# Kernel tuning notes

Hardware: AMD Instinct MI355X
Metric: run time of the kernel (lower is better)

Reference implementation:

```python
import jax, jax.numpy as jnp
import numpy as np
import math

MODEL_DIM = 1024
NUM_HEADS = 16
ATTN_DIM = MODEL_DIM // NUM_HEADS  # 64
ROWS, COLS, AXES = 32, 32, 2
PAIRS = ATTN_DIM // (AXES * 2)     # 16
BATCH = 4
TOKENS = ROWS * COLS               # 1024


def setup_inputs() -> dict:
    key = jax.random.key(0)
    ks = jax.random.split(key, 8)
    s = 1.0 / math.sqrt(MODEL_DIM)
    return {
        "x": jax.random.normal(ks[0], (BATCH, TOKENS, MODEL_DIM), jnp.float32),
        "cos": jax.random.uniform(ks[1], (ROWS, COLS, AXES, PAIRS), jnp.float32),
        "sin": jax.random.uniform(ks[2], (ROWS, COLS, AXES, PAIRS), jnp.float32),
        "Wq": jax.random.normal(ks[3], (MODEL_DIM, MODEL_DIM), jnp.float32) * s,
        "Wk": jax.random.normal(ks[4], (MODEL_DIM, MODEL_DIM), jnp.float32) * s,
        "Wv": jax.random.normal(ks[5], (MODEL_DIM, MODEL_DIM), jnp.float32) * s,
        "Wo": jax.random.normal(ks[6], (MODEL_DIM, MODEL_DIM), jnp.float32) * s,
        "bo": jax.random.normal(ks[7], (MODEL_DIM,), jnp.float32) * 0.01,
    }


def _apply_rope(W, cos, sin):
    # W: (b, h, tokens, attn_dim) -> (b, h, rows, cols, axes, pairs, 2)
    b, h, n, d = W.shape
    rows, cols, axes, pairs = cos.shape
    Wp = W.reshape(b, h, rows, cols, axes, pairs, 2)
    c = cos[None, None]
    s = sin[None, None]
    w0, w1 = Wp[..., 0], Wp[..., 1]
    out = jnp.stack([c * w0 - s * w1, s * w0 + c * w1], axis=-1)
    return out.reshape(b, h, n, d)


def reference(x, cos, sin, Wq, Wk, Wv, Wo, bo):
    b, n, _ = x.shape
    # torch Linear: y = x @ W.T
    Q = (x @ Wq.T).reshape(b, n, NUM_HEADS, ATTN_DIM).transpose(0, 2, 1, 3)
    K = (x @ Wk.T).reshape(b, n, NUM_HEADS, ATTN_DIM).transpose(0, 2, 1, 3)
    V = (x @ Wv.T).reshape(b, n, NUM_HEADS, ATTN_DIM).transpose(0, 2, 1, 3)
    Q = _apply_rope(Q, cos, sin)
    K = _apply_rope(K, cos, sin)
    scores = jnp.einsum("bhqd,bhkd->bhqk", Q, K) / math.sqrt(ATTN_DIM)
    attn = jax.nn.softmax(scores, axis=-1)
    o = jnp.einsum("bhqk,bhkd->bhqd", attn, V)
    o = o.transpose(0, 2, 1, 3).reshape(b, n, MODEL_DIM)
    return o @ Wo.T + bo
```

## Files before the change

### kernel.cpp

```cpp
#include <hip/hip_runtime.h>
#include <hip/hip_bf16.h>

typedef __bf16 bf16;
typedef __bf16 bf16x4 __attribute__((ext_vector_type(4)));
typedef __bf16 bf16x8 __attribute__((ext_vector_type(8)));
typedef float  f32x4  __attribute__((ext_vector_type(4)));
typedef unsigned int u32x2 __attribute__((ext_vector_type(2)));

#define MFMA16(a, b, c) __builtin_amdgcn_mfma_f32_16x16x32_bf16((a), (b), (c), 0, 0, 0)

#define GLOBAL_AS(p) ((const __attribute__((address_space(1))) void*)(p))
#define LDS_AS(p)    ((__attribute__((address_space(3))) void*)(p))

#define BATCH 4
#define TOK   1024
#define DIM   1024
#define HEADS 16
#define HD    64
#define MTOT  (BATCH * TOK)
#define MELEM (1024u * 1024u)

__global__ __launch_bounds__(256) void k_cast(const float* __restrict__ X,
                                              bf16* __restrict__ xh)
{
    size_t i0 = ((size_t)blockIdx.x * 256 + threadIdx.x) * 8;
    f32x4 a = *(const f32x4*)(X + i0);
    f32x4 b = *(const f32x4*)(X + i0 + 4);
    bf16x8 h;
    #pragma unroll
    for (int j = 0; j < 4; j++) { h[j] = (bf16)a[j]; h[4 + j] = (bf16)b[j]; }
    *(bf16x8*)(xh + i0) = h;
}

__global__ __launch_bounds__(256) void k_split(
    const float* __restrict__ W0, const float* __restrict__ W1,
    const float* __restrict__ W2, const float* __restrict__ W3,
    bf16* __restrict__ wsp)
{
    const int widx = blockIdx.y;
    const float* W = (widx == 0) ? W0 : (widx == 1) ? W1 : (widx == 2) ? W2 : W3;
    size_t i0 = ((size_t)blockIdx.x * 256 + threadIdx.x) * 8;
    f32x4 a = *(const f32x4*)(W + i0);
    f32x4 b = *(const f32x4*)(W + i0 + 4);
    bf16x8 h, l;
    #pragma unroll
    for (int j = 0; j < 4; j++) {
        bf16 g0 = (bf16)a[j]; h[j] = g0;     l[j] = (bf16)(a[j] - (float)g0);
        bf16 g1 = (bf16)b[j]; h[4 + j] = g1; l[4 + j] = (bf16)(b[j] - (float)g1);
    }
    *(bf16x8*)(wsp + (size_t)widx * MELEM + i0) = h;
    if (widx == 3)
        *(bf16x8*)(wsp + 4 * (size_t)MELEM + i0) = l;
}

__global__ __launch_bounds__(512) void k_gemmQKV(
    const bf16* __restrict__ Ag, const bf16* __restrict__ wsp,
    const float* __restrict__ cosT, const float* __restrict__ sinT,
    bf16* __restrict__ q_o, bf16* __restrict__ k_o, bf16* __restrict__ v_o)
{
    __shared__ bf16 Alin[128 * 64];
    __shared__ bf16 Blin[256 * 64];

    const int fid = blockIdx.x;
    const int swz = (fid & 7) * 48 + (fid >> 3);
    const int nt = swz % 12;
    const int mt = swz / 12;

    const int t = threadIdx.x;
    const int lane = t & 63;
    const int w = t >> 6;
    const int wr = w >> 2, wc = w & 3;
    const int l15 = lane & 15;

    f32x4 acc[4][4];
    #pragma unroll
    for (int m = 0; m < 4; m++)
        #pragma unroll
        for (int n = 0; n < 4; n++)
            #pragma unroll
            for (int r = 0; r < 4; r++) acc[m][n][r] = 0.f;

    const int srow = lane >> 3;
    const int schk8 = ((lane & 7) ^ (srow & 7)) * 8;
    const bf16* asrc = Ag  + (size_t)(mt * 128 + srow) * DIM + schk8;
    const bf16* bsrc = wsp + (size_t)(nt * 256 + srow) * DIM + schk8;

    for (int k0 = 0; k0 < DIM; k0 += 64) {
        __syncthreads();
        #pragma unroll
        for (int ii = 0; ii < 2; ++ii) {
            int i = w * 2 + ii;
            __builtin_amdgcn_global_load_lds(
                GLOBAL_AS(asrc + (size_t)i * 8 * DIM + k0),
                LDS_AS(&Alin[i * 512]), 16, 0, 0);
        }
        #pragma unroll
        for (int jj = 0; jj < 4; ++jj) {
            int j = w * 4 + jj;
            __builtin_amdgcn_global_load_lds(
                GLOBAL_AS(bsrc + (size_t)j * 8 * DIM + k0),
                LDS_AS(&Blin[j * 512]), 16, 0, 0);
        }
        __syncthreads();

        #pragma unroll
        for (int ks = 0; ks < 2; ks++) {
            const int cc = (lane >> 4) + ks * 4;
            bf16x8 fb[4];
            #pragma unroll
            for (int n = 0; n < 4; n++) {
                int rb = wc * 64 + n * 16 + l15;
                fb[n] = *(const bf16x8*)&Blin[rb * 64 + ((cc ^ (rb & 7)) << 3)];
            }
            #pragma unroll
            for (int m = 0; m < 4; m++) {
                int r = wr * 64 + m * 16 + l15;
                bf16x8 fa = *(const bf16x8*)&Alin[r * 64 + ((cc ^ (r & 7)) << 3)];
                #pragma unroll
                for (int n = 0; n < 4; n++)
                    acc[m][n] = MFMA16(fa, fb[n], acc[m][n]);
            }
        }
    }

    const int mode = nt >> 2;
    const int h = (nt & 3) * 4 + wc;
    if (mode == 2) {
        #pragma unroll
        for (int m = 0; m < 4; m++) {
            const int grow0 = mt * 128 + wr * 64 + m * 16 + (lane >> 4) * 4;
            const int b = grow0 >> 10, ntok0 = grow0 & (TOK - 1);
            #pragma unroll
            for (int n = 0; n < 4; n++) {
                const int d = n * 16 + l15;
                bf16x4 pk;
                #pragma unroll
                for (int r = 0; r < 4; r++) pk[r] = (bf16)acc[m][n][r];
                *(bf16x4*)&v_o[((size_t)((b * HEADS + h) * HD + d)) * TOK + ntok0] = pk;
            }
        }
    } else {
        __syncthreads();
        float* cosL = (float*)Alin;
        float* sinL = (float*)Blin;
        const int tb = (mt & 7) * 128;
        *(f32x4*)(cosL + t * 8)     = *(const f32x4*)(cosT + (size_t)tb * 32 + t * 8);
        *(f32x4*)(cosL + t * 8 + 4) = *(const f32x4*)(cosT + (size_t)tb * 32 + t * 8 + 4);
        *(f32x4*)(sinL + t * 8)     = *(const f32x4*)(sinT + (size_t)tb * 32 + t * 8);
        *(f32x4*)(sinL + t * 8 + 4) = *(const f32x4*)(sinT + (size_t)tb * 32 + t * 8 + 4);
        __syncthreads();

        bf16* dst = (mode == 0) ? q_o : k_o;
        const float sc = (mode == 0) ? 0.125f : 1.0f;
        #pragma unroll
        for (int m = 0; m < 4; m++) {
            const int grow0 = mt * 128 + wr * 64 + m * 16 + (lane >> 4) * 4;
            const int b = grow0 >> 10, ntok0 = grow0 & (TOK - 1);
            const int loc0 = wr * 64 + m * 16 + (lane >> 4) * 4;
            #pragma unroll
            for (int n = 0; n < 4; n++) {
                const int d = n * 16 + l15;
                const int idp = (d >> 5) * 16 + ((d >> 1) & 15);
                const bool ev = (d & 1) == 0;
                #pragma unroll
                for (int r = 0; r < 4; r++) {
                    float v = acc[m][n][r];
                    float pr = __shfl_xor(v, 1, 64);
                    float c = cosL[(loc0 + r) * 32 + idp];
                    float s = sinL[(loc0 + r) * 32 + idp];
                    float res = (ev ? (c * v - s * pr) : (s * pr + c * v)) * sc;
                    dst[((size_t)(b * HEADS + h) * TOK + ntok0 + r) * HD + d] = (bf16)res;
                }
            }
        }
    }
}

__global__ __launch_bounds__(256) void k_gemmO(
    const bf16* __restrict__ Ag, const bf16* __restrict__ wsp,
    const float* __restrict__ bo, float* __restrict__ f_o)
{
    __shared__ bf16 Alin[128 * 64];
    __shared__ bf16 Bhlin[128 * 64];
    __shared__ bf16 Bllin[128 * 64];

    const bf16* Bh_g = wsp + 3 * (size_t)MELEM;
    const bf16* Bl_g = wsp + 4 * (size_t)MELEM;

    const int fid = blockIdx.x;
    const int swz = (fid & 7) * 32 + (fid >> 3);
    const int nt = swz & 7;
    const int mt = swz >> 3;

    const int t = threadIdx.x;
    const int lane = t & 63;
    const int w = t >> 6;
    const int wr = w >> 1, wc = w & 1;

    f32x4 acc[4][4];
    #pragma unroll
    for (int m = 0; m < 4; m++)
        #pragma unroll
        for (int n = 0; n < 4; n++)
            #pragma unroll
            for (int r = 0; r < 4; r++) acc[m][n][r] = 0.f;

    const int srow = lane >> 3;
    const int schk8 = ((lane & 7) ^ (srow & 7)) * 8;
    const bf16* asrc  = Ag   + (size_t)(mt * 128 + srow) * DIM + schk8;
    const bf16* bhsrc = Bh_g + (size_t)(nt * 128 + srow) * DIM + schk8;
    const bf16* blsrc = Bl_g + (size_t)(nt * 128 + srow) * DIM + schk8;

    for (int k0 = 0; k0 < DIM; k0 += 64) {
        __syncthreads();
        #pragma unroll
        for (int ii = 0; ii < 4; ++ii) {
            int i = w * 4 + ii;
            size_t roff = (size_t)i * 8 * DIM + k0;
            __builtin_amdgcn_global_load_lds(GLOBAL_AS(asrc + roff),
                                             LDS_AS(&Alin[i * 512]), 16, 0, 0);
            __builtin_amdgcn_global_load_lds(GLOBAL_AS(bhsrc + roff),
                                             LDS_AS(&Bhlin[i * 512]), 16, 0, 0);
            __builtin_amdgcn_global_load_lds(GLOBAL_AS(blsrc + roff),
                                             LDS_AS(&Bllin[i * 512]), 16, 0, 0);
        }
        __syncthreads();

        const int l15 = lane & 15;
        #pragma unroll
        for (int ks = 0; ks < 2; ks++) {
            const int cc = (lane >> 4) + ks * 4;
            bf16x8 fbh[4], fbl[4];
            #pragma unroll
            for (int n = 0; n < 4; n++) {
                int r = wc * 64 + n * 16 + l15;
                int off = r * 64 + ((cc ^ (r & 7)) << 3);
                fbh[n] = *(const bf16x8*)&Bhlin[off];
                fbl[n] = *(const bf16x8*)&Bllin[off];
            }
            #pragma unroll
            for (int m = 0; m < 4; m++) {
                int r = wr * 64 + m * 16 + l15;
                bf16x8 fa = *(const bf16x8*)&Alin[r * 64 + ((cc ^ (r & 7)) << 3)];
                #pragma unroll
                for (int n = 0; n < 4; n++) {
                    acc[m][n] = MFMA16(fa, fbh[n], acc[m][n]);
                    acc[m][n] = MFMA16(fa, fbl[n], acc[m][n]);
                }
            }
        }
    }

    #pragma unroll
    for (int m = 0; m < 4; m++) {
        #pragma unroll
        for (int n = 0; n < 4; n++) {
            const int grow0 = mt * 128 + wr * 64 + m * 16 + (lane >> 4) * 4;
            const int gcol  = nt * 128 + wc * 64 + n * 16 + (lane & 15);
            const float bias = bo[gcol];
            #pragma unroll
            for (int r = 0; r < 4; r++)
                f_o[(size_t)(grow0 + r) * DIM + gcol] = acc[m][n][r] + bias;
        }
    }
}

__global__ __launch_bounds__(256) void k_attn(
    const bf16* __restrict__ Q, const bf16* __restrict__ K,
    const bf16* __restrict__ Vt, bf16* __restrict__ O)
{
    __shared__ bf16 Ks[128 * 64];
    __shared__ bf16 Vs[64 * 128];
    __shared__ bf16 Ps[64 * 128];

    const int fid = blockIdx.x;
    const int swz = (fid & 7) * 128 + (fid >> 3);
    const int qt = swz & 15;
    const int bh = swz >> 4;

    const int t = threadIdx.x;
    const int lane = t & 63;
    const int w = t >> 6;
    const int col = lane & 15;
    const int grp = lane >> 4;

    const bf16* qp = Q + ((size_t)bh * TOK + qt * 64 + w * 16 + col) * HD + grp * 8;
    bf16x8 qf0 = *(const bf16x8*)qp;
    bf16x8 qf1 = *(const bf16x8*)(qp + 32);

    const bf16* ksrc = K + ((size_t)bh * TOK + (lane >> 3)) * HD
                         + (size_t)(((lane & 7) ^ ((lane >> 3) & 7)) * 8);
    const bf16* vbase = Vt + ((size_t)bh * HD + grp) * TOK;
    const bf16* vsrc_e = vbase + (size_t)(((lane & 15) ^ grp) * 8);
    const bf16* vsrc_o = vbase + (size_t)(((lane & 15) ^ (grp + 4)) * 8);

    float l_sum = 0.f;
    f32x4 zero = {0.f, 0.f, 0.f, 0.f};
    f32x4 o_[4];
    #pragma unroll
    for (int dt = 0; dt < 4; dt++) o_[dt] = zero;

    unsigned int* PsU = (unsigned int*)Ps;
    const int m7 = col & 7;

    for (int kt = 0; kt < 8; kt++) {
        __syncthreads();
        #pragma unroll
        for (int ii = 0; ii < 4; ++ii) {
            int i = w * 4 + ii;
            __builtin_amdgcn_global_load_lds(
                GLOBAL_AS(ksrc + (size_t)(kt * 128 + i * 8) * HD),
                LDS_AS(&Ks[i * 512]), 16, 0, 0);
            const bf16* vs = (i & 1) ? vsrc_o : vsrc_e;
            __builtin_amdgcn_global_load_lds(
                GLOBAL_AS(vs + (size_t)i * 4 * TOK + kt * 128),
                LDS_AS(&Vs[i * 512]), 16, 0, 0);
        }
        __syncthreads();

        f32x4 s[8];
        #pragma unroll
        for (int ct = 0; ct < 8; ct++) s[ct] = zero;
        #pragma unroll
        for (int ct = 0; ct < 8; ct++) {
            int rbase = (ct * 16 + col) * 64;
            bf16x8 kf0 = *(const bf16x8*)&Ks[rbase + ((grp ^ m7) << 3)];
            bf16x8 kf1 = *(const bf16x8*)&Ks[rbase + (((grp + 4) ^ m7) << 3)];
            s[ct] = MFMA16(kf0, qf0, s[ct]);
            s[ct] = MFMA16(kf1, qf1, s[ct]);
        }

        const int qrow = w * 16 + col;
        #pragma unroll
        for (int ct = 0; ct < 8; ct++) {
            float p0 = exp2f(s[ct][0] * 1.44269504f - 23.0831206f);
            float p1 = exp2f(s[ct][1] * 1.44269504f - 23.0831206f);
            float p2 = exp2f(s[ct][2] * 1.44269504f - 23.0831206f);
            float p3 = exp2f(s[ct][3] * 1.44269504f - 23.0831206f);
            l_sum += (p0 + p1) + (p2 + p3);
            unsigned int a0, a1;
            asm("v_cvt_pk_bf16_f32 %0, %1, %2" : "=v"(a0) : "v"(p0), "v"(p1));
            asm("v_cvt_pk_bf16_f32 %0, %1, %2" : "=v"(a1) : "v"(p2), "v"(p3));
            int cs = (2 * ct + (grp >> 1)) ^ m7;
            u32x2 st = {a0, a1};
            *(u32x2*)&PsU[qrow * 64 + cs * 4 + (grp & 1) * 2] = st;
        }

        #pragma unroll
        for (int tt = 0; tt < 4; tt++) {
            bf16x8 pf = *(const bf16x8*)&Ps[qrow * 128 + (((4 * tt + grp) ^ m7) << 3)];
            #pragma unroll
            for (int dt = 0; dt < 4; dt++) {
                bf16x8 vf = *(const bf16x8*)&Vs[(dt * 16 + col) * 128
                                                + (((4 * tt + grp) ^ m7) << 3)];
                o_[dt] = MFMA16(vf, pf, o_[dt]);
            }
        }
    }

    l_sum += __shfl_xor(l_sum, 16, 64);
    l_sum += __shfl_xor(l_sum, 32, 64);
    const float inv = 1.0f / l_sum;

    const int b = bh >> 4, h = bh & 15;
    const int ntok = qt * 64 + w * 16 + col;
    #pragma unroll
    for (int dt = 0; dt < 4; dt++) {
        bf16x4 pk4;
        #pragma unroll
        for (int r = 0; r < 4; r++) pk4[r] = (bf16)(o_[dt][r] * inv);
        *(bf16x4*)&O[((size_t)b * TOK + ntok) * DIM + h * HD + dt * 16 + grp * 4] = pk4;
    }
}

extern "C" void kernel_launch(void* const* d_in, const int* in_sizes, int n_in,
                              void* d_out, int out_size, void* d_ws, size_t ws_size,
                              hipStream_t stream)
{
    const float* x    = (const float*)d_in[0];
    const float* cosT = (const float*)d_in[1];
    const float* sinT = (const float*)d_in[2];
    const float* Wq   = (const float*)d_in[3];
    const float* Wk   = (const float*)d_in[4];
    const float* Wv   = (const float*)d_in[5];
    const float* Wo   = (const float*)d_in[6];
    const float* bo   = (const float*)d_in[7];
    float* out = (float*)d_out;

    bf16* xh  = (bf16*)d_ws;
    bf16* qw  = xh + 4 * (size_t)MELEM;
    bf16* kw  = qw + 4 * (size_t)MELEM;
    bf16* vw  = kw + 4 * (size_t)MELEM;
    bf16* wsp = vw + 4 * (size_t)MELEM;
    bf16* ow  = xh;

    k_cast<<<dim3(2048), dim3(256), 0, stream>>>(x, xh);
    k_split<<<dim3(512, 4), dim3(256), 0, stream>>>(Wq, Wk, Wv, Wo, wsp);
    k_gemmQKV<<<dim3(384), dim3(512), 0, stream>>>(xh, wsp, cosT, sinT, qw, kw, vw);
    k_attn<<<dim3(1024), dim3(256), 0, stream>>>(qw, kw, vw, ow);
    k_gemmO<<<dim3(256), dim3(256), 0, stream>>>(ow, wsp, bo, out);
}
```

Baseline: 114.3 us.

## Double attention query tile per block and merge cast/split prep kernels

```diff
diff --git a/kernel.cpp b/kernel.cpp
--- a/kernel.cpp
+++ b/kernel.cpp
@@ -20,37 +20,39 @@
 #define MTOT  (BATCH * TOK)
 #define MELEM (1024u * 1024u)
 
-__global__ __launch_bounds__(256) void k_cast(const float* __restrict__ X,
-                                              bf16* __restrict__ xh)
-{
-    size_t i0 = ((size_t)blockIdx.x * 256 + threadIdx.x) * 8;
-    f32x4 a = *(const f32x4*)(X + i0);
-    f32x4 b = *(const f32x4*)(X + i0 + 4);
-    bf16x8 h;
-    #pragma unroll
-    for (int j = 0; j < 4; j++) { h[j] = (bf16)a[j]; h[4 + j] = (bf16)b[j]; }
-    *(bf16x8*)(xh + i0) = h;
-}
-
-__global__ __launch_bounds__(256) void k_split(
+__global__ __launch_bounds__(256) void k_prep(
+    const float* __restrict__ X,
     const float* __restrict__ W0, const float* __restrict__ W1,
     const float* __restrict__ W2, const float* __restrict__ W3,
-    bf16* __restrict__ wsp)
+    bf16* __restrict__ xh, bf16* __restrict__ wsp)
 {
-    const int widx = blockIdx.y;
-    const float* W = (widx == 0) ? W0 : (widx == 1) ? W1 : (widx == 2) ? W2 : W3;
-    size_t i0 = ((size_t)blockIdx.x * 256 + threadIdx.x) * 8;
-    f32x4 a = *(const f32x4*)(W + i0);
-    f32x4 b = *(const f32x4*)(W + i0 + 4);
-    bf16x8 h, l;
-    #pragma unroll
-    for (int j = 0; j < 4; j++) {
-        bf16 g0 = (bf16)a[j]; h[j] = g0;     l[j] = (bf16)(a[j] - (float)g0);
-        bf16 g1 = (bf16)b[j]; h[4 + j] = g1; l[4 + j] = (bf16)(b[j] - (float)g1);
-    }
-    *(bf16x8*)(wsp + (size_t)widx * MELEM + i0) = h;
-    if (widx == 3)
-        *(bf16x8*)(wsp + 4 * (size_t)MELEM + i0) = l;
+    const int bid = blockIdx.x;
+    if (bid < 2048) {
+        size_t i0 = ((size_t)bid * 256 + threadIdx.x) * 8;
+        f32x4 a = *(const f32x4*)(X + i0);
+        f32x4 b = *(const f32x4*)(X + i0 + 4);
+        bf16x8 h;
+        #pragma unroll
+        for (int j = 0; j < 4; j++) { h[j] = (bf16)a[j]; h[4 + j] = (bf16)b[j]; }
+        *(bf16x8*)(xh + i0) = h;
+    } else {
+        const int b2 = bid - 2048;
+        const int widx = b2 >> 9;
+        const int inner = b2 & 511;
+        const float* W = (widx == 0) ? W0 : (widx == 1) ? W1 : (widx == 2) ? W2 : W3;
+        size_t i0 = ((size_t)inner * 256 + threadIdx.x) * 8;
+        f32x4 a = *(const f32x4*)(W + i0);
+        f32x4 b = *(const f32x4*)(W + i0 + 4);
+        bf16x8 h, l;
+        #pragma unroll
+        for (int j = 0; j < 4; j++) {
+            bf16 g0 = (bf16)a[j]; h[j] = g0;     l[j] = (bf16)(a[j] - (float)g0);
+            bf16 g1 = (bf16)b[j]; h[4 + j] = g1; l[4 + j] = (bf16)(b[j] - (float)g1);
+        }
+        *(bf16x8*)(wsp + (size_t)widx * MELEM + i0) = h;
+        if (widx == 3)
+            *(bf16x8*)(wsp + 4 * (size_t)MELEM + i0) = l;
+    }
 }
 
 __global__ __launch_bounds__(512) void k_gemmQKV(
@@ -271,22 +273,26 @@
 {
     __shared__ bf16 Ks[128 * 64];
     __shared__ bf16 Vs[64 * 128];
-    __shared__ bf16 Ps[64 * 128];
+    __shared__ bf16 Ps[128 * 128];
 
     const int fid = blockIdx.x;
-    const int swz = (fid & 7) * 128 + (fid >> 3);
-    const int qt = swz & 15;
-    const int bh = swz >> 4;
+    const int swz = (fid & 7) * 64 + (fid >> 3);
+    const int qt = swz & 7;
+    const int bh = swz >> 3;
 
     const int t = threadIdx.x;
     const int lane = t & 63;
     const int w = t >> 6;
     const int col = lane & 15;
     const int grp = lane >> 4;
-
-    const bf16* qp = Q + ((size_t)bh * TOK + qt * 64 + w * 16 + col) * HD + grp * 8;
-    bf16x8 qf0 = *(const bf16x8*)qp;
-    bf16x8 qf1 = *(const bf16x8*)(qp + 32);
+    const int m7 = col & 7;
+    const int qrow = w * 16 + col;
+
+    const bf16* qp0 = Q + ((size_t)bh * TOK + qt * 128 + qrow) * HD + grp * 8;
+    bf16x8 qa0 = *(const bf16x8*)qp0;
+    bf16x8 qb0 = *(const bf16x8*)(qp0 + 32);
+    bf16x8 qa1 = *(const bf16x8*)(qp0 + 64 * HD);
+    bf16x8 qb1 = *(const bf16x8*)(qp0 + 64 * HD + 32);
 
     const bf16* ksrc = K + ((size_t)bh * TOK + (lane >> 3)) * HD
                          + (size_t)(((lane & 7) ^ ((lane >> 3) & 7)) * 8);
@@ -294,14 +300,13 @@
     const bf16* vsrc_e = vbase + (size_t)(((lane & 15) ^ grp) * 8);
     const bf16* vsrc_o = vbase + (size_t)(((lane & 15) ^ (grp + 4)) * 8);
 
-    float l_sum = 0.f;
+    float l0 = 0.f, l1 = 0.f;
     f32x4 zero = {0.f, 0.f, 0.f, 0.f};
-    f32x4 o_[4];
+    f32x4 oA[4], oB[4];
     #pragma unroll
-    for (int dt = 0; dt < 4; dt++) o_[dt] = zero;
+    for (int dt = 0; dt < 4; dt++) { oA[dt] = zero; oB[dt] = zero; }
 
     unsigned int* PsU = (unsigned int*)Ps;
-    const int m7 = col & 7;
 
     for (int kt = 0; kt < 8; kt++) {
         __syncthreads();
@@ -318,58 +323,94 @@
         }
         __syncthreads();
 
-        f32x4 s[8];
-        #pragma unroll
-        for (int ct = 0; ct < 8; ct++) s[ct] = zero;
-        #pragma unroll
-        for (int ct = 0; ct < 8; ct++) {
-            int rbase = (ct * 16 + col) * 64;
-            bf16x8 kf0 = *(const bf16x8*)&Ks[rbase + ((grp ^ m7) << 3)];
-            bf16x8 kf1 = *(const bf16x8*)&Ks[rbase + (((grp + 4) ^ m7) << 3)];
-            s[ct] = MFMA16(kf0, qf0, s[ct]);
-            s[ct] = MFMA16(kf1, qf1, s[ct]);
-        }
-
-        const int qrow = w * 16 + col;
-        #pragma unroll
-        for (int ct = 0; ct < 8; ct++) {
-            float p0 = exp2f(s[ct][0] * 1.44269504f - 23.0831206f);
-            float p1 = exp2f(s[ct][1] * 1.44269504f - 23.0831206f);
-            float p2 = exp2f(s[ct][2] * 1.44269504f - 23.0831206f);
-            float p3 = exp2f(s[ct][3] * 1.44269504f - 23.0831206f);
-            l_sum += (p0 + p1) + (p2 + p3);
-            unsigned int a0, a1;
-            asm("v_cvt_pk_bf16_f32 %0, %1, %2" : "=v"(a0) : "v"(p0), "v"(p1));
-            asm("v_cvt_pk_bf16_f32 %0, %1, %2" : "=v"(a1) : "v"(p2), "v"(p3));
-            int cs = (2 * ct + (grp >> 1)) ^ m7;
-            u32x2 st = {a0, a1};
-            *(u32x2*)&PsU[qrow * 64 + cs * 4 + (grp & 1) * 2] = st;
+        {
+            f32x4 s[8];
+            #pragma unroll
+            for (int ct = 0; ct < 8; ct++) s[ct] = zero;
+            #pragma unroll
+            for (int ct = 0; ct < 8; ct++) {
+                int rbase = (ct * 16 + col) * 64;
+                bf16x8 kf0 = *(const bf16x8*)&Ks[rbase + ((grp ^ m7) << 3)];
+                bf16x8 kf1 = *(const bf16x8*)&Ks[rbase + (((grp + 4) ^ m7) << 3)];
+                s[ct] = MFMA16(kf0, qa0, s[ct]);
+                s[ct] = MFMA16(kf1, qb0, s[ct]);
+            }
+            #pragma unroll
+            for (int ct = 0; ct < 8; ct++) {
+                float p0 = exp2f(s[ct][0] * 1.44269504f - 23.0831206f);
+                float p1 = exp2f(s[ct][1] * 1.44269504f - 23.0831206f);
+                float p2 = exp2f(s[ct][2] * 1.44269504f - 23.0831206f);
+                float p3 = exp2f(s[ct][3] * 1.44269504f - 23.0831206f);
+                l0 += (p0 + p1) + (p2 + p3);
+                unsigned int a0, a1;
+                asm("v_cvt_pk_bf16_f32 %0, %1, %2" : "=v"(a0) : "v"(p0), "v"(p1));
+                asm("v_cvt_pk_bf16_f32 %0, %1, %2" : "=v"(a1) : "v"(p2), "v"(p3));
+                int cs = (2 * ct + (grp >> 1)) ^ m7;
+                u32x2 st = {a0, a1};
+                *(u32x2*)&PsU[qrow * 64 + cs * 4 + (grp & 1) * 2] = st;
+            }
+        }
+        {
+            f32x4 s[8];
+            #pragma unroll
+            for (int ct = 0; ct < 8; ct++) s[ct] = zero;
+            #pragma unroll
+            for (int ct = 0; ct < 8; ct++) {
+                int rbase = (ct * 16 + col) * 64;
+                bf16x8 kf0 = *(const bf16x8*)&Ks[rbase + ((grp ^ m7) << 3)];
+                bf16x8 kf1 = *(const bf16x8*)&Ks[rbase + (((grp + 4) ^ m7) << 3)];
+                s[ct] = MFMA16(kf0, qa1, s[ct]);
+                s[ct] = MFMA16(kf1, qb1, s[ct]);
+            }
+            #pragma unroll
+            for (int ct = 0; ct < 8; ct++) {
+                float p0 = exp2f(s[ct][0] * 1.44269504f - 23.0831206f);
+                float p1 = exp2f(s[ct][1] * 1.44269504f - 23.0831206f);
+                float p2 = exp2f(s[ct][2] * 1.44269504f - 23.0831206f);
+                float p3 = exp2f(s[ct][3] * 1.44269504f - 23.0831206f);
+                l1 += (p0 + p1) + (p2 + p3);
+                unsigned int a0, a1;
+                asm("v_cvt_pk_bf16_f32 %0, %1, %2" : "=v"(a0) : "v"(p0), "v"(p1));
+                asm("v_cvt_pk_bf16_f32 %0, %1, %2" : "=v"(a1) : "v"(p2), "v"(p3));
+                int cs = (2 * ct + (grp >> 1)) ^ m7;
+                u32x2 st = {a0, a1};
+                *(u32x2*)&PsU[(64 + qrow) * 64 + cs * 4 + (grp & 1) * 2] = st;
+            }
         }
 
         #pragma unroll
         for (int tt = 0; tt < 4; tt++) {
-            bf16x8 pf = *(const bf16x8*)&Ps[qrow * 128 + (((4 * tt + grp) ^ m7) << 3)];
+            const int coff = ((4 * tt + grp) ^ m7) << 3;
+            bf16x8 pfA = *(const bf16x8*)&Ps[qrow * 128 + coff];
+            bf16x8 pfB = *(const bf16x8*)&Ps[(64 + qrow) * 128 + coff];
             #pragma unroll
             for (int dt = 0; dt < 4; dt++) {
-                bf16x8 vf = *(const bf16x8*)&Vs[(dt * 16 + col) * 128
-                                                + (((4 * tt + grp) ^ m7) << 3)];
-                o_[dt] = MFMA16(vf, pf, o_[dt]);
-            }
-        }
-    }
-
-    l_sum += __shfl_xor(l_sum, 16, 64);
-    l_sum += __shfl_xor(l_sum, 32, 64);
-    const float inv = 1.0f / l_sum;
+                bf16x8 vf = *(const bf16x8*)&Vs[(dt * 16 + col) * 128 + coff];
+                oA[dt] = MFMA16(vf, pfA, oA[dt]);
+                oB[dt] = MFMA16(vf, pfB, oB[dt]);
+            }
+        }
+    }
+
+    l0 += __shfl_xor(l0, 16, 64);
+    l0 += __shfl_xor(l0, 32, 64);
+    l1 += __shfl_xor(l1, 16, 64);
+    l1 += __shfl_xor(l1, 32, 64);
+    const float inv0 = 1.0f / l0;
+    const float inv1 = 1.0f / l1;
 
     const int b = bh >> 4, h = bh & 15;
-    const int ntok = qt * 64 + w * 16 + col;
+    const int nt0 = qt * 128 + qrow;
     #pragma unroll
     for (int dt = 0; dt < 4; dt++) {
-        bf16x4 pk4;
-        #pragma unroll
-        for (int r = 0; r < 4; r++) pk4[r] = (bf16)(o_[dt][r] * inv);
-        *(bf16x4*)&O[((size_t)b * TOK + ntok) * DIM + h * HD + dt * 16 + grp * 4] = pk4;
+        bf16x4 pkA, pkB;
+        #pragma unroll
+        for (int r = 0; r < 4; r++) {
+            pkA[r] = (bf16)(oA[dt][r] * inv0);
+            pkB[r] = (bf16)(oB[dt][r] * inv1);
+        }
+        *(bf16x4*)&O[((size_t)b * TOK + nt0) * DIM + h * HD + dt * 16 + grp * 4] = pkA;
+        *(bf16x4*)&O[((size_t)b * TOK + nt0 + 64) * DIM + h * HD + dt * 16 + grp * 4] = pkB;
     }
 }
 
@@ -394,9 +435,8 @@
     bf16* wsp = vw + 4 * (size_t)MELEM;
     bf16* ow  = xh;
 
-    k_cast<<<dim3(2048), dim3(256), 0, stream>>>(x, xh);
-    k_split<<<dim3(512, 4), dim3(256), 0, stream>>>(Wq, Wk, Wv, Wo, wsp);
+    k_prep<<<dim3(4096), dim3(256), 0, stream>>>(x, Wq, Wk, Wv, Wo, xh, wsp);
     k_gemmQKV<<<dim3(384), dim3(512), 0, stream>>>(xh, wsp, cosT, sinT, qw, kw, vw);
-    k_attn<<<dim3(1024), dim3(256), 0, stream>>>(qw, kw, vw, ow);
+    k_attn<<<dim3(512), dim3(256), 0, stream>>>(qw, kw, vw, ow);
     k_gemmO<<<dim3(256), dim3(256), 0, stream>>>(ow, wsp, bo, out);
 }
```

New measurement: 107.1 us. 1.07x faster.

## Double-buffer K/V tiles in attention and merge cast/split prep kernels

Applied to the files above, without the earlier changes.

```diff
diff --git a/kernel.cpp b/kernel.cpp
--- a/kernel.cpp
+++ b/kernel.cpp
@@ -20,37 +20,39 @@
 #define MTOT  (BATCH * TOK)
 #define MELEM (1024u * 1024u)
 
-__global__ __launch_bounds__(256) void k_cast(const float* __restrict__ X,
-                                              bf16* __restrict__ xh)
-{
-    size_t i0 = ((size_t)blockIdx.x * 256 + threadIdx.x) * 8;
-    f32x4 a = *(const f32x4*)(X + i0);
-    f32x4 b = *(const f32x4*)(X + i0 + 4);
-    bf16x8 h;
-    #pragma unroll
-    for (int j = 0; j < 4; j++) { h[j] = (bf16)a[j]; h[4 + j] = (bf16)b[j]; }
-    *(bf16x8*)(xh + i0) = h;
-}
-
-__global__ __launch_bounds__(256) void k_split(
+__global__ __launch_bounds__(256) void k_prep(
+    const float* __restrict__ X,
     const float* __restrict__ W0, const float* __restrict__ W1,
     const float* __restrict__ W2, const float* __restrict__ W3,
-    bf16* __restrict__ wsp)
+    bf16* __restrict__ xh, bf16* __restrict__ wsp)
 {
-    const int widx = blockIdx.y;
-    const float* W = (widx == 0) ? W0 : (widx == 1) ? W1 : (widx == 2) ? W2 : W3;
-    size_t i0 = ((size_t)blockIdx.x * 256 + threadIdx.x) * 8;
-    f32x4 a = *(const f32x4*)(W + i0);
-    f32x4 b = *(const f32x4*)(W + i0 + 4);
-    bf16x8 h, l;
-    #pragma unroll
-    for (int j = 0; j < 4; j++) {
-        bf16 g0 = (bf16)a[j]; h[j] = g0;     l[j] = (bf16)(a[j] - (float)g0);
-        bf16 g1 = (bf16)b[j]; h[4 + j] = g1; l[4 + j] = (bf16)(b[j] - (float)g1);
-    }
-    *(bf16x8*)(wsp + (size_t)widx * MELEM + i0) = h;
-    if (widx == 3)
-        *(bf16x8*)(wsp + 4 * (size_t)MELEM + i0) = l;
+    const int bid = blockIdx.x;
+    if (bid < 2048) {
+        size_t i0 = ((size_t)bid * 256 + threadIdx.x) * 8;
+        f32x4 a = *(const f32x4*)(X + i0);
+        f32x4 b = *(const f32x4*)(X + i0 + 4);
+        bf16x8 h;
+        #pragma unroll
+        for (int j = 0; j < 4; j++) { h[j] = (bf16)a[j]; h[4 + j] = (bf16)b[j]; }
+        *(bf16x8*)(xh + i0) = h;
+    } else {
+        const int b2 = bid - 2048;
+        const int widx = b2 >> 9;
+        const int inner = b2 & 511;
+        const float* W = (widx == 0) ? W0 : (widx == 1) ? W1 : (widx == 2) ? W2 : W3;
+        size_t i0 = ((size_t)inner * 256 + threadIdx.x) * 8;
+        f32x4 a = *(const f32x4*)(W + i0);
+        f32x4 b = *(const f32x4*)(W + i0 + 4);
+        bf16x8 h, l;
+        #pragma unroll
+        for (int j = 0; j < 4; j++) {
+            bf16 g0 = (bf16)a[j]; h[j] = g0;     l[j] = (bf16)(a[j] - (float)g0);
+            bf16 g1 = (bf16)b[j]; h[4 + j] = g1; l[4 + j] = (bf16)(b[j] - (float)g1);
+        }
+        *(bf16x8*)(wsp + (size_t)widx * MELEM + i0) = h;
+        if (widx == 3)
+            *(bf16x8*)(wsp + 4 * (size_t)MELEM + i0) = l;
+    }
 }
 
 __global__ __launch_bounds__(512) void k_gemmQKV(
@@ -269,9 +271,9 @@
     const bf16* __restrict__ Q, const bf16* __restrict__ K,
     const bf16* __restrict__ Vt, bf16* __restrict__ O)
 {
-    __shared__ bf16 Ks[128 * 64];
-    __shared__ bf16 Vs[64 * 128];
-    __shared__ bf16 Ps[64 * 128];
+    __shared__ bf16 Ks[2][64 * 64];
+    __shared__ bf16 Vs[2][64 * 64];
+    __shared__ bf16 Ps[64 * 64];
 
     const int fid = blockIdx.x;
     const int swz = (fid & 7) * 128 + (fid >> 3);
@@ -283,16 +285,17 @@
     const int w = t >> 6;
     const int col = lane & 15;
     const int grp = lane >> 4;
-
-    const bf16* qp = Q + ((size_t)bh * TOK + qt * 64 + w * 16 + col) * HD + grp * 8;
+    const int m7 = col & 7;
+    const int qrow = w * 16 + col;
+
+    const bf16* qp = Q + ((size_t)bh * TOK + qt * 64 + qrow) * HD + grp * 8;
     bf16x8 qf0 = *(const bf16x8*)qp;
     bf16x8 qf1 = *(const bf16x8*)(qp + 32);
 
-    const bf16* ksrc = K + ((size_t)bh * TOK + (lane >> 3)) * HD
-                         + (size_t)(((lane & 7) ^ ((lane >> 3) & 7)) * 8);
-    const bf16* vbase = Vt + ((size_t)bh * HD + grp) * TOK;
-    const bf16* vsrc_e = vbase + (size_t)(((lane & 15) ^ grp) * 8);
-    const bf16* vsrc_o = vbase + (size_t)(((lane & 15) ^ (grp + 4)) * 8);
+    const int srow = lane >> 3;
+    const int schk8 = ((lane & 7) ^ (srow & 7)) * 8;
+    const bf16* ksrc = K  + ((size_t)bh * TOK + srow) * HD + schk8;
+    const bf16* vsrc = Vt + ((size_t)bh * HD + srow) * TOK + schk8;
 
     float l_sum = 0.f;
     f32x4 zero = {0.f, 0.f, 0.f, 0.f};
@@ -301,38 +304,40 @@
     for (int dt = 0; dt < 4; dt++) o_[dt] = zero;
 
     unsigned int* PsU = (unsigned int*)Ps;
-    const int m7 = col & 7;
-
-    for (int kt = 0; kt < 8; kt++) {
-        __syncthreads();
-        #pragma unroll
-        for (int ii = 0; ii < 4; ++ii) {
-            int i = w * 4 + ii;
+
+    auto stage = [&](int kt, int b) {
+        #pragma unroll
+        for (int ii = 0; ii < 2; ++ii) {
+            int i = w * 2 + ii;
             __builtin_amdgcn_global_load_lds(
-                GLOBAL_AS(ksrc + (size_t)(kt * 128 + i * 8) * HD),
-                LDS_AS(&Ks[i * 512]), 16, 0, 0);
-            const bf16* vs = (i & 1) ? vsrc_o : vsrc_e;
+                GLOBAL_AS(ksrc + (size_t)(kt * 64 + i * 8) * HD),
+                LDS_AS(&Ks[b][i * 512]), 16, 0, 0);
             __builtin_amdgcn_global_load_lds(
-                GLOBAL_AS(vs + (size_t)i * 4 * TOK + kt * 128),
-                LDS_AS(&Vs[i * 512]), 16, 0, 0);
-        }
-        __syncthreads();
-
-        f32x4 s[8];
-        #pragma unroll
-        for (int ct = 0; ct < 8; ct++) s[ct] = zero;
-        #pragma unroll
-        for (int ct = 0; ct < 8; ct++) {
+                GLOBAL_AS(vsrc + (size_t)(i * 8) * TOK + kt * 64),
+                LDS_AS(&Vs[b][i * 512]), 16, 0, 0);
+        }
+    };
+
+    stage(0, 0);
+    for (int kt = 0; kt < 16; kt++) {
+        const int buf = kt & 1;
+        __syncthreads();
+        if (kt < 15) stage(kt + 1, buf ^ 1);
+
+        f32x4 s[4];
+        #pragma unroll
+        for (int ct = 0; ct < 4; ct++) s[ct] = zero;
+        #pragma unroll
+        for (int ct = 0; ct < 4; ct++) {
             int rbase = (ct * 16 + col) * 64;
-            bf16x8 kf0 = *(const bf16x8*)&Ks[rbase + ((grp ^ m7) << 3)];
-            bf16x8 kf1 = *(const bf16x8*)&Ks[rbase + (((grp + 4) ^ m7) << 3)];
+            bf16x8 kf0 = *(const bf16x8*)&Ks[buf][rbase + ((grp ^ m7) << 3)];
+            bf16x8 kf1 = *(const bf16x8*)&Ks[buf][rbase + (((grp + 4) ^ m7) << 3)];
             s[ct] = MFMA16(kf0, qf0, s[ct]);
             s[ct] = MFMA16(kf1, qf1, s[ct]);
         }
 
-        const int qrow = w * 16 + col;
-        #pragma unroll
-        for (int ct = 0; ct < 8; ct++) {
+        #pragma unroll
+        for (int ct = 0; ct < 4; ct++) {
             float p0 = exp2f(s[ct][0] * 1.44269504f - 23.0831206f);
             float p1 = exp2f(s[ct][1] * 1.44269504f - 23.0831206f);
             float p2 = exp2f(s[ct][2] * 1.44269504f - 23.0831206f);
@@ -343,16 +348,16 @@
             asm("v_cvt_pk_bf16_f32 %0, %1, %2" : "=v"(a1) : "v"(p2), "v"(p3));
             int cs = (2 * ct + (grp >> 1)) ^ m7;
             u32x2 st = {a0, a1};
-            *(u32x2*)&PsU[qrow * 64 + cs * 4 + (grp & 1) * 2] = st;
-        }
-
-        #pragma unroll
-        for (int tt = 0; tt < 4; tt++) {
-            bf16x8 pf = *(const bf16x8*)&Ps[qrow * 128 + (((4 * tt + grp) ^ m7) << 3)];
+            *(u32x2*)&PsU[qrow * 32 + cs * 4 + (grp & 1) * 2] = st;
+        }
+
+        #pragma unroll
+        for (int tt = 0; tt < 2; tt++) {
+            const int coff = ((4 * tt + grp) ^ m7) << 3;
+            bf16x8 pf = *(const bf16x8*)&Ps[qrow * 64 + coff];
             #pragma unroll
             for (int dt = 0; dt < 4; dt++) {
-                bf16x8 vf = *(const bf16x8*)&Vs[(dt * 16 + col) * 128
-                                                + (((4 * tt + grp) ^ m7) << 3)];
+                bf16x8 vf = *(const bf16x8*)&Vs[buf][(dt * 16 + col) * 64 + coff];
                 o_[dt] = MFMA16(vf, pf, o_[dt]);
             }
         }
@@ -363,7 +368,7 @@
     const float inv = 1.0f / l_sum;
 
     const int b = bh >> 4, h = bh & 15;
-    const int ntok = qt * 64 + w * 16 + col;
+    const int ntok = qt * 64 + qrow;
     #pragma unroll
     for (int dt = 0; dt < 4; dt++) {
         bf16x4 pk4;
@@ -394,8 +399,7 @@
     bf16* wsp = vw + 4 * (size_t)MELEM;
     bf16* ow  = xh;
 
-    k_cast<<<dim3(2048), dim3(256), 0, stream>>>(x, xh);
-    k_split<<<dim3(512, 4), dim3(256), 0, stream>>>(Wq, Wk, Wv, Wo, wsp);
+    k_prep<<<dim3(4096), dim3(256), 0, stream>>>(x, Wq, Wk, Wv, Wo, xh, wsp);
     k_gemmQKV<<<dim3(384), dim3(512), 0, stream>>>(xh, wsp, cosT, sinT, qw, kw, vw);
     k_attn<<<dim3(1024), dim3(256), 0, stream>>>(qw, kw, vw, ow);
     k_gemmO<<<dim3(256), dim3(256), 0, stream>>>(ow, wsp, bo, out);
```

Result: faster. 108.3 us (-5.3%).
